# Optimization experiments

Measured on AMD Instinct MI355X. Metric: run time of the kernel, lower is better.

## Reference

```python
import jax, jax.numpy as jnp
import numpy as np

IGNORE_INDEX = -100

def reference(output, labels):
    # output: [B, C, D, H, W] logits; labels: [B, 1, D, H, W] int
    C = output.shape[1]
    logits = jnp.transpose(output, (0, 2, 3, 4, 1)).reshape(-1, C)  # [N, C]
    lab = labels.transpose(0, 2, 3, 4, 1).reshape(-1)               # [N]
    # per-element cross-entropy (reduce=False)
    logp = jax.nn.log_softmax(logits, axis=-1)                      # [N, C]
    losses = -jnp.take_along_axis(logp, lab[:, None], axis=-1)[:, 0]  # [N]
    # per-class sums and counts in one scatter-add pass
    sums = jax.ops.segment_sum(losses, lab, num_segments=C)         # [C]
    counts = jax.ops.segment_sum(jnp.ones_like(losses), lab, num_segments=C)
    present = counts > 0                                            # class has samples
    class_means = sums / jnp.maximum(counts, 1.0)
    n_valid = jnp.sum(present.astype(losses.dtype))
    loss_mean = jnp.sum(jnp.where(present, class_means, 0.0)) / n_valid
    return loss_mean

def setup_inputs() -> dict:
    key = jax.random.key(0)
    k1, k2 = jax.random.split(key)
    B, C, D, H, W = 4, 8, 64, 128, 128
    output = jax.random.normal(k1, (B, C, D, H, W), dtype=jnp.float32)
    labels = jax.random.randint(k2, (B, 1, D, H, W), 0, C, dtype=jnp.int64)
    return {"output": output, "labels": labels}
```

## Files before the change

kernel.cpp:

```cpp
#include <hip/hip_runtime.h>

#define NC 8
#define SPATIAL_LOG2 20
#define SPATIAL (1 << SPATIAL_LOG2)
#define NVEC (4 * SPATIAL / 4)
#define NBLK (NVEC / 256)
#define NSLOT 256
#define LOG2E 1.4426950408889634f
#define LN2   0.6931471805599453f


__global__ void ce_init(float* __restrict__ ws) {
    const int i = blockIdx.x * 256 + threadIdx.x;
    if (i < 16 * NSLOT) ws[i] = 0.0f;
}

__global__ __launch_bounds__(256) void ce_main(const float* __restrict__ logits,
                                               const int* __restrict__ labels,
                                               float* __restrict__ ws) {
    const int v = blockIdx.x * 256 + threadIdx.x;
    const int n0 = v << 2;
    const int b = n0 >> SPATIAL_LOG2;
    const int s = n0 & (SPATIAL - 1);

    const int4 lab4 = *reinterpret_cast<const int4*>(labels + n0);
    const int labs[4] = {lab4.x, lab4.y, lab4.z, lab4.w};

    const float* base = logits + (((size_t)b * NC) << SPATIAL_LOG2) + s;
    float4 x[NC];
#pragma unroll
    for (int c = 0; c < NC; ++c)
        x[c] = *reinterpret_cast<const float4*>(base + ((size_t)c << SPATIAL_LOG2));

    float lsum[NC];
#pragma unroll
    for (int c = 0; c < NC; ++c) lsum[c] = 0.0f;
    unsigned int wcnt[NC];
#pragma unroll
    for (int c = 0; c < NC; ++c) wcnt[c] = 0u;

#pragma unroll
    for (int j = 0; j < 4; ++j) {
        float xj[NC];
#pragma unroll
        for (int c = 0; c < NC; ++c)
            xj[c] = reinterpret_cast<const float*>(&x[c])[j];

        const int lab = labs[j];
        float sum = 0.0f, xl = 0.0f;
#pragma unroll
        for (int c = 0; c < NC; ++c) {
            sum += exp2f(xj[c] * LOG2E);
            xl = (lab == c) ? xj[c] : xl;
        }
        const float loss = log2f(sum) * LN2 - xl;

#pragma unroll
        for (int c = 0; c < NC; ++c) {
            const bool e = (lab == c);
            lsum[c] += e ? loss : 0.0f;
            wcnt[c] += (unsigned)__popcll(__ballot(e));
        }
    }

#pragma unroll
    for (int c = 0; c < NC; ++c) {
#pragma unroll
        for (int off = 32; off > 0; off >>= 1)
            lsum[c] += __shfl_xor(lsum[c], off);
    }

    __shared__ float bsum[NC];
    __shared__ unsigned int bcnt[NC];
    if (threadIdx.x < NC) { bsum[threadIdx.x] = 0.0f; bcnt[threadIdx.x] = 0u; }
    __syncthreads();

    if ((threadIdx.x & 63) == 0) {
#pragma unroll
        for (int c = 0; c < NC; ++c) {
            atomicAdd(&bsum[c], lsum[c]);
            atomicAdd(&bcnt[c], wcnt[c]);
        }
    }
    __syncthreads();

    const int slot = blockIdx.x & (NSLOT - 1);
    if (threadIdx.x < NC)
        atomicAdd(&ws[threadIdx.x * NSLOT + slot], bsum[threadIdx.x]);
    else if (threadIdx.x < 2 * NC)
        atomicAdd(&ws[threadIdx.x * NSLOT + slot], (float)bcnt[threadIdx.x - NC]);
}

__global__ void ce_final(const float* __restrict__ ws, float* __restrict__ out) {
    const int w = threadIdx.x >> 6;
    const int lane = threadIdx.x & 63;
    __shared__ float fin[16];
#pragma unroll
    for (int k = 0; k < 4; ++k) {
        const int c = w * 4 + k;
        float vsum = ws[c * NSLOT + lane] + ws[c * NSLOT + lane + 64] +
                     ws[c * NSLOT + lane + 128] + ws[c * NSLOT + lane + 192];
#pragma unroll
        for (int off = 32; off > 0; off >>= 1)
            vsum += __shfl_xor(vsum, off);
        if (lane == 0) fin[c] = vsum;
    }
    __syncthreads();
    if (threadIdx.x == 0) {
        float tot = 0.0f, npres = 0.0f;
#pragma unroll
        for (int c = 0; c < NC; ++c) {
            const float cnt = fin[NC + c];
            if (cnt > 0.0f) { tot += fin[c] / cnt; npres += 1.0f; }
        }
        out[0] = tot / npres;
    }
}

extern "C" void kernel_launch(void* const* d_in, const int* in_sizes, int n_in,
                              void* d_out, int out_size, void* d_ws, size_t ws_size,
                              hipStream_t stream) {
    const float* logits = (const float*)d_in[0];
    const int* labels = (const int*)d_in[1];
    float* out = (float*)d_out;
    float* ws = (float*)d_ws;

    ce_init<<<16, 256, 0, stream>>>(ws);
    ce_main<<<NBLK, 256, 0, stream>>>(logits, labels, ws);
    ce_final<<<1, 256, 0, stream>>>(ws, out);
}
```

Measured before the change: 42.64 us.

## Replace global atomics with per-block partial writes and drop init kernel

Each block now reduces its waves' partial sums and counts through a shared array and writes 16 values to a per-block slot in the workspace, instead of using shared and global atomics. Because every slot is overwritten, the zeroing kernel is removed, leaving two launches instead of three. Block size doubles to 512 threads (2048 blocks), and the final kernel uses 1024 threads with float4 loads to sum 2048 partials per quantity. This removes atomic contention and one launch, at the cost of a larger final reduction.

```diff
diff --git a/kernel.cpp b/kernel.cpp
--- a/kernel.cpp
+++ b/kernel.cpp
@@ -3,22 +3,16 @@
 #define NC 8
 #define SPATIAL_LOG2 20
 #define SPATIAL (1 << SPATIAL_LOG2)
-#define NVEC (4 * SPATIAL / 4)
-#define NBLK (NVEC / 256)
-#define NSLOT 256
+#define TPB 512
+#define NBLK 2048
 #define LOG2E 1.4426950408889634f
 #define LN2   0.6931471805599453f
 
 
-__global__ void ce_init(float* __restrict__ ws) {
-    const int i = blockIdx.x * 256 + threadIdx.x;
-    if (i < 16 * NSLOT) ws[i] = 0.0f;
-}
-
-__global__ __launch_bounds__(256) void ce_main(const float* __restrict__ logits,
+__global__ __launch_bounds__(TPB) void ce_main(const float* __restrict__ logits,
                                                const int* __restrict__ labels,
                                                float* __restrict__ ws) {
-    const int v = blockIdx.x * 256 + threadIdx.x;
+    const int v = blockIdx.x * TPB + threadIdx.x;
     const int n0 = v << 2;
     const int b = n0 >> SPATIAL_LOG2;
     const int s = n0 & (SPATIAL - 1);
@@ -70,42 +64,42 @@
             lsum[c] += __shfl_xor(lsum[c], off);
     }
 
-    __shared__ float bsum[NC];
-    __shared__ unsigned int bcnt[NC];
-    if (threadIdx.x < NC) { bsum[threadIdx.x] = 0.0f; bcnt[threadIdx.x] = 0u; }
-    __syncthreads();
-
+    __shared__ float part[TPB / 64][16];
+    const int w = threadIdx.x >> 6;
     if ((threadIdx.x & 63) == 0) {
 #pragma unroll
         for (int c = 0; c < NC; ++c) {
-            atomicAdd(&bsum[c], lsum[c]);
-            atomicAdd(&bcnt[c], wcnt[c]);
+            part[w][c] = lsum[c];
+            part[w][NC + c] = (float)wcnt[c];
         }
     }
     __syncthreads();
 
-    const int slot = blockIdx.x & (NSLOT - 1);
-    if (threadIdx.x < NC)
-        atomicAdd(&ws[threadIdx.x * NSLOT + slot], bsum[threadIdx.x]);
-    else if (threadIdx.x < 2 * NC)
-        atomicAdd(&ws[threadIdx.x * NSLOT + slot], (float)bcnt[threadIdx.x - NC]);
+    if (threadIdx.x < 16) {
+        float acc = 0.0f;
+#pragma unroll
+        for (int w2 = 0; w2 < TPB / 64; ++w2) acc += part[w2][threadIdx.x];
+        ws[threadIdx.x * NBLK + blockIdx.x] = acc;
+    }
 }
 
-__global__ void ce_final(const float* __restrict__ ws, float* __restrict__ out) {
+__global__ __launch_bounds__(1024) void ce_final(const float* __restrict__ ws,
+                                                 float* __restrict__ out) {
     const int w = threadIdx.x >> 6;
     const int lane = threadIdx.x & 63;
     __shared__ float fin[16];
+
+    float acc = 0.0f;
 #pragma unroll
-    for (int k = 0; k < 4; ++k) {
-        const int c = w * 4 + k;
-        float vsum = ws[c * NSLOT + lane] + ws[c * NSLOT + lane + 64] +
-                     ws[c * NSLOT + lane + 128] + ws[c * NSLOT + lane + 192];
+    for (int k = 0; k < NBLK / 256; ++k) {
+        const float4 p = *reinterpret_cast<const float4*>(ws + w * NBLK + k * 256 + lane * 4);
+        acc += p.x + p.y + p.z + p.w;
+    }
 #pragma unroll
-        for (int off = 32; off > 0; off >>= 1)
-            vsum += __shfl_xor(vsum, off);
-        if (lane == 0) fin[c] = vsum;
-    }
+    for (int off = 32; off > 0; off >>= 1) acc += __shfl_xor(acc, off);
+    if (lane == 0) fin[w] = acc;
     __syncthreads();
+
     if (threadIdx.x == 0) {
         float tot = 0.0f, npres = 0.0f;
 #pragma unroll
@@ -125,7 +119,6 @@
     float* out = (float*)d_out;
     float* ws = (float*)d_ws;
 
-    ce_init<<<16, 256, 0, stream>>>(ws);
-    ce_main<<<NBLK, 256, 0, stream>>>(logits, labels, ws);
-    ce_final<<<1, 256, 0, stream>>>(ws, out);
+    ce_main<<<NBLK, TPB, 0, stream>>>(logits, labels, ws);
+    ce_final<<<1, 1024, 0, stream>>>(ws, out);
 }
```

After: 35.42 us, median of 2. 1.2x faster.
